# Performance work log

Hardware: AMD Instinct MI355X
Metric: run time of the kernel (lower is better)

The kernel has to match this reference:

```python
import jax, jax.numpy as jnp
import numpy as np

D_K = 64

def setup_inputs() -> dict:
    key = jax.random.key(0)
    k1, k2, k3 = jax.random.split(key, 3)
    B, H, S, d = 4, 16, 2048, D_K
    Q = jax.random.normal(k1, (B, H, S, d), dtype=jnp.float32)
    K = jax.random.normal(k2, (B, H, S, d), dtype=jnp.float32)
    V = jax.random.normal(k3, (B, H, S, d), dtype=jnp.float32)
    attn_mask = jnp.ones((1, 1, S, S), dtype=jnp.float32)
    return {"Q": Q, "K": K, "V": V, "attn_mask": attn_mask}

def reference(Q, K, V, attn_mask):
    # scores = Q K^T / sqrt(d_k)  -> [B, H, S, S]
    scale = 1.0 / np.sqrt(D_K).astype(np.float32)
    scores = jnp.einsum('bhqd,bhkd->bhqk', Q, K) * scale
    # unnormalized exp (NO max-subtraction, faithful to original)
    scores = jnp.exp(scores)
    # multiplicative mask applied POST-exp
    scores = scores * attn_mask
    # manual sum-normalization with eps
    attn = scores / (jnp.sum(scores, axis=-1, keepdims=True) + 1e-08)
    context = jnp.einsum('bhqk,bhkd->bhqd', attn, V)
    return (context, attn)
```

## Files before the change

### kernel.cpp

```cpp
#include <hip/hip_runtime.h>

#define S_LEN 2048
#define D_KD  64
#define NKT   32
#define NBH   64
#define KSEG  4

typedef __attribute__((ext_vector_type(8))) short short8;
typedef __attribute__((ext_vector_type(4))) float f32x4;

__device__ __forceinline__ unsigned short f2bf(float f) {
    unsigned u = __builtin_bit_cast(unsigned, f);
    return (unsigned short)((u + 0x7fffu + ((u >> 16) & 1u)) >> 16);
}

__device__ __forceinline__ unsigned swz(int row, int bytecol) {
    return (unsigned)(row * 128 + bytecol) ^
           (((((unsigned)row & 7u) ^ ((unsigned)row >> 3)) & 7u) << 4);
}

__device__ __forceinline__ void load_rm(const float* __restrict__ g,
                                        float4 r[4], int tid) {
#pragma unroll
    for (int j = 0; j < 4; j++) r[j] = *(const float4*)(g + j * 1024 + tid * 4);
}
__device__ __forceinline__ void write_rm(const float4 r[4],
                                         unsigned char* lds, int tid) {
#pragma unroll
    for (int j = 0; j < 4; j++) {
        int idx = j * 1024 + tid * 4;
        int row = idx >> 6, col = idx & 63;
        ushort4 b = make_ushort4(f2bf(r[j].x), f2bf(r[j].y), f2bf(r[j].z), f2bf(r[j].w));
        *(ushort4*)(lds + swz(row, col * 2)) = b;
    }
}
__device__ __forceinline__ void load_tr(const float* __restrict__ g,
                                        float4 r[4], int tid) {
    const int br = tid >> 4, bc = tid & 15;
    const float* gp = g + (4 * br) * 64 + 4 * bc;
#pragma unroll
    for (int j = 0; j < 4; j++) r[j] = *(const float4*)(gp + j * 64);
}
__device__ __forceinline__ void write_tr(const float4 r[4],
                                         unsigned char* lds, int tid) {
    const int br = tid >> 4, bc = tid & 15;
    ushort4 c;
    c = make_ushort4(f2bf(r[0].x), f2bf(r[1].x), f2bf(r[2].x), f2bf(r[3].x));
    *(ushort4*)(lds + swz(4 * bc + 0, 8 * br)) = c;
    c = make_ushort4(f2bf(r[0].y), f2bf(r[1].y), f2bf(r[2].y), f2bf(r[3].y));
    *(ushort4*)(lds + swz(4 * bc + 1, 8 * br)) = c;
    c = make_ushort4(f2bf(r[0].z), f2bf(r[1].z), f2bf(r[2].z), f2bf(r[3].z));
    *(ushort4*)(lds + swz(4 * bc + 2, 8 * br)) = c;
    c = make_ushort4(f2bf(r[0].w), f2bf(r[1].w), f2bf(r[2].w), f2bf(r[3].w));
    *(ushort4*)(lds + swz(4 * bc + 3, 8 * br)) = c;
}

__device__ __forceinline__ void stage_rm(const float* __restrict__ g,
                                         unsigned char* lds, int tid) {
    float4 r[4];
    load_rm(g, r, tid);
    write_rm(r, lds, tid);
}

__device__ __forceinline__ void qkt(const unsigned char* Qs, const unsigned char* Ks,
                                    int wv, int lr, int lg, f32x4 acc[4]) {
    short8 a0 = *(const short8*)(Qs + swz(16 * wv + lr, 16 * lg));
    short8 a1 = *(const short8*)(Qs + swz(16 * wv + lr, 16 * lg + 64));
#pragma unroll
    for (int nt = 0; nt < 4; nt++) {
        short8 b0 = *(const short8*)(Ks + swz(16 * nt + lr, 16 * lg));
        short8 b1 = *(const short8*)(Ks + swz(16 * nt + lr, 16 * lg + 64));
        acc[nt] = __builtin_amdgcn_mfma_f32_16x16x32_bf16(a0, b0, acc[nt], 0, 0, 0);
        acc[nt] = __builtin_amdgcn_mfma_f32_16x16x32_bf16(a1, b1, acc[nt], 0, 0, 0);
    }
}

__global__ __launch_bounds__(256) void attn_ctx(
    const float* __restrict__ Q, const float* __restrict__ K,
    const float* __restrict__ V, const float* __restrict__ M,
    float* __restrict__ out, float* __restrict__ invg) {
    __shared__ unsigned char Qs[8192];
    __shared__ unsigned char Ks[8192];
    __shared__ unsigned char Vs[8192];
    __shared__ unsigned char Ps[8192];

    const int tid = threadIdx.x;
    const int wv = tid >> 6, lane = tid & 63, lr = lane & 15, lg = lane >> 4;
    const int qt = blockIdx.x & 31, bh = blockIdx.x >> 5;

    const float* Qg = Q + ((size_t)bh * S_LEN + qt * 64) * D_KD;
    const float* Kg = K + (size_t)bh * S_LEN * D_KD;
    const float* Vg = V + (size_t)bh * S_LEN * D_KD;
    float* ctxg = out + ((size_t)bh * S_LEN + qt * 64) * D_KD;
    const float* Mg = M + (size_t)(qt * 64) * S_LEN;

    stage_rm(Qg, Qs, tid);

    f32x4 accc[4] = {};
    float rs[4] = {0.f, 0.f, 0.f, 0.f};

    float4 kreg[4], vreg[4];
    load_rm(Kg, kreg, tid);
    load_tr(Vg, vreg, tid);

    for (int t = 0; t < NKT; t++) {
        write_rm(kreg, Ks, tid);
        write_tr(vreg, Vs, tid);
        __syncthreads();

        if (t + 1 < NKT) {
            load_rm(Kg + (size_t)(t + 1) * 64 * D_KD, kreg, tid);
            load_tr(Vg + (size_t)(t + 1) * 64 * D_KD, vreg, tid);
        }

        f32x4 acc[4] = {};
        qkt(Qs, Ks, wv, lr, lg, acc);

#pragma unroll
        for (int r = 0; r < 4; r++) {
            const int row = 16 * wv + 4 * lg + r;
            const float* mrow = Mg + (size_t)row * S_LEN + t * 64;
#pragma unroll
            for (int nt = 0; nt < 4; nt++) {
                float e = __expf(acc[nt][r] * 0.125f) * mrow[16 * nt + lr];
                rs[r] += e;
                *(unsigned short*)(Ps + swz(row, (16 * nt + lr) * 2)) = f2bf(e);
            }
        }
        __syncthreads();

#pragma unroll
        for (int kt = 0; kt < 2; kt++) {
            short8 pa = *(const short8*)(Ps + swz(16 * wv + lr, 16 * lg + 64 * kt));
#pragma unroll
            for (int nt = 0; nt < 4; nt++) {
                short8 vb = *(const short8*)(Vs + swz(16 * nt + lr, 16 * lg + 64 * kt));
                accc[nt] = __builtin_amdgcn_mfma_f32_16x16x32_bf16(pa, vb, accc[nt], 0, 0, 0);
            }
        }
        __syncthreads();
    }

    float inv[4];
#pragma unroll
    for (int r = 0; r < 4; r++) {
        float v = rs[r];
        v += __shfl_xor(v, 1);
        v += __shfl_xor(v, 2);
        v += __shfl_xor(v, 4);
        v += __shfl_xor(v, 8);
        inv[r] = 1.0f / (v + 1e-8f);
    }

#pragma unroll
    for (int r = 0; r < 4; r++) {
        const int row = 16 * wv + 4 * lg + r;
#pragma unroll
        for (int nt = 0; nt < 4; nt++)
            ctxg[(size_t)row * D_KD + 16 * nt + lr] = accc[nt][r] * inv[r];
    }

    if (lr == 0) {
#pragma unroll
        for (int r = 0; r < 4; r++)
            invg[(size_t)bh * S_LEN + qt * 64 + 16 * wv + 4 * lg + r] = inv[r];
    }
}

__global__ __launch_bounds__(256) void attn_mat(
    const float* __restrict__ Q, const float* __restrict__ K,
    const float* __restrict__ M, const float* __restrict__ invg,
    float* __restrict__ out) {
    __shared__ unsigned char Qs[8192];
    __shared__ unsigned char Ks[8192];

    const int tid = threadIdx.x;
    const int wv = tid >> 6, lane = tid & 63, lr = lane & 15, lg = lane >> 4;
    const int ks = blockIdx.x & (KSEG - 1);
    const int qt = (blockIdx.x >> 2) & 31;
    const int bh = blockIdx.x >> 7;

    const float* Qg = Q + ((size_t)bh * S_LEN + qt * 64) * D_KD;
    const float* Kg = K + (size_t)bh * S_LEN * D_KD;
    const float* Mg = M + (size_t)(qt * 64) * S_LEN;
    float* attng = out + (size_t)NBH * S_LEN * D_KD +
                   (size_t)bh * S_LEN * S_LEN + (size_t)(qt * 64) * S_LEN;

    stage_rm(Qg, Qs, tid);

    float inv[4];
#pragma unroll
    for (int r = 0; r < 4; r++)
        inv[r] = invg[(size_t)bh * S_LEN + qt * 64 + 16 * wv + 4 * lg + r];

    const int nt_kt = S_LEN / (64 * KSEG);
    for (int kt = 0; kt < nt_kt; kt++) {
        const int key0 = ks * (S_LEN / KSEG) + kt * 64;
        if (kt) __syncthreads();
        stage_rm(Kg + (size_t)key0 * D_KD, Ks, tid);
        __syncthreads();

        f32x4 acc[4] = {};
        qkt(Qs, Ks, wv, lr, lg, acc);

#pragma unroll
        for (int r = 0; r < 4; r++) {
            const int row = 16 * wv + 4 * lg + r;
            const float* mrow = Mg + (size_t)row * S_LEN + key0;
            float* arow = attng + (size_t)row * S_LEN + key0;
#pragma unroll
            for (int nt = 0; nt < 4; nt++) {
                float e = __expf(acc[nt][r] * 0.125f) * mrow[16 * nt + lr] * inv[r];
                __builtin_nontemporal_store(e, arow + 16 * nt + lr);
            }
        }
    }
}

extern "C" void kernel_launch(void* const* d_in, const int* in_sizes, int n_in,
                              void* d_out, int out_size, void* d_ws, size_t ws_size,
                              hipStream_t stream) {
    const float* Q = (const float*)d_in[0];
    const float* K = (const float*)d_in[1];
    const float* V = (const float*)d_in[2];
    const float* M = (const float*)d_in[3];
    float* out = (float*)d_out;
    float* invg = (float*)d_ws;
    attn_ctx<<<dim3(NBH * 32), dim3(256), 0, stream>>>(Q, K, V, M, out, invg);
    attn_mat<<<dim3(NBH * 32 * KSEG), dim3(256), 0, stream>>>(Q, K, M, invg, out);
}
```

Before: 496.1 us.

## Prefetch K and mask tiles into registers and use LDS-only barriers

Replaces __syncthreads with a barrier that waits only on LDS counters, so in-flight global prefetches are not drained at each barrier. Mask values are loaded into registers before the QK^T MFMAs so their latency overlaps compute. The attention-matrix kernel gains register double-buffering of K tiles, matching the context kernel. This costs extra registers per thread, which may reduce occupancy.

```diff
diff --git a/kernel.cpp b/kernel.cpp
--- a/kernel.cpp
+++ b/kernel.cpp
@@ -12,6 +12,11 @@
 __device__ __forceinline__ unsigned short f2bf(float f) {
     unsigned u = __builtin_bit_cast(unsigned, f);
     return (unsigned short)((u + 0x7fffu + ((u >> 16) & 1u)) >> 16);
+}
+
+__device__ __forceinline__ void ldsbar() {
+    asm volatile("s_waitcnt lgkmcnt(0)" ::: "memory");
+    __builtin_amdgcn_s_barrier();
 }
 
 __device__ __forceinline__ unsigned swz(int row, int bytecol) {
@@ -106,28 +111,35 @@
     for (int t = 0; t < NKT; t++) {
         write_rm(kreg, Ks, tid);
         write_tr(vreg, Vs, tid);
-        __syncthreads();
+        ldsbar();
 
         if (t + 1 < NKT) {
             load_rm(Kg + (size_t)(t + 1) * 64 * D_KD, kreg, tid);
             load_tr(Vg + (size_t)(t + 1) * 64 * D_KD, vreg, tid);
         }
 
+        float mreg[4][4];
+#pragma unroll
+        for (int r = 0; r < 4; r++) {
+            const float* mrow = Mg + (size_t)(16 * wv + 4 * lg + r) * S_LEN + t * 64;
+#pragma unroll
+            for (int nt = 0; nt < 4; nt++) mreg[r][nt] = mrow[16 * nt + lr];
+        }
+
         f32x4 acc[4] = {};
         qkt(Qs, Ks, wv, lr, lg, acc);
 
 #pragma unroll
         for (int r = 0; r < 4; r++) {
             const int row = 16 * wv + 4 * lg + r;
-            const float* mrow = Mg + (size_t)row * S_LEN + t * 64;
 #pragma unroll
             for (int nt = 0; nt < 4; nt++) {
-                float e = __expf(acc[nt][r] * 0.125f) * mrow[16 * nt + lr];
+                float e = __expf(acc[nt][r] * 0.125f) * mreg[r][nt];
                 rs[r] += e;
                 *(unsigned short*)(Ps + swz(row, (16 * nt + lr) * 2)) = f2bf(e);
             }
         }
-        __syncthreads();
+        ldsbar();
 
 #pragma unroll
         for (int kt = 0; kt < 2; kt++) {
@@ -138,7 +150,7 @@
                 accc[nt] = __builtin_amdgcn_mfma_f32_16x16x32_bf16(pa, vb, accc[nt], 0, 0, 0);
             }
         }
-        __syncthreads();
+        ldsbar();
     }
 
     float inv[4];
@@ -194,11 +206,26 @@
         inv[r] = invg[(size_t)bh * S_LEN + qt * 64 + 16 * wv + 4 * lg + r];
 
     const int nt_kt = S_LEN / (64 * KSEG);
+    const float* Kseg = Kg + (size_t)(ks * (S_LEN / KSEG)) * D_KD;
+
+    float4 kreg[4];
+    load_rm(Kseg, kreg, tid);
+
     for (int kt = 0; kt < nt_kt; kt++) {
         const int key0 = ks * (S_LEN / KSEG) + kt * 64;
-        if (kt) __syncthreads();
-        stage_rm(Kg + (size_t)key0 * D_KD, Ks, tid);
-        __syncthreads();
+        write_rm(kreg, Ks, tid);
+        ldsbar();
+
+        if (kt + 1 < nt_kt)
+            load_rm(Kseg + (size_t)(kt + 1) * 64 * D_KD, kreg, tid);
+
+        float mreg[4][4];
+#pragma unroll
+        for (int r = 0; r < 4; r++) {
+            const float* mrow = Mg + (size_t)(16 * wv + 4 * lg + r) * S_LEN + key0;
+#pragma unroll
+            for (int nt = 0; nt < 4; nt++) mreg[r][nt] = mrow[16 * nt + lr];
+        }
 
         f32x4 acc[4] = {};
         qkt(Qs, Ks, wv, lr, lg, acc);
@@ -206,14 +233,14 @@
 #pragma unroll
         for (int r = 0; r < 4; r++) {
             const int row = 16 * wv + 4 * lg + r;
-            const float* mrow = Mg + (size_t)row * S_LEN + key0;
             float* arow = attng + (size_t)row * S_LEN + key0;
 #pragma unroll
             for (int nt = 0; nt < 4; nt++) {
-                float e = __expf(acc[nt][r] * 0.125f) * mrow[16 * nt + lr] * inv[r];
+                float e = __expf(acc[nt][r] * 0.125f) * mreg[r][nt] * inv[r];
                 __builtin_nontemporal_store(e, arow + 16 * nt + lr);
             }
         }
+        ldsbar();
     }
 }
 
```

Result: faster. 461.3 us (-7.0%).
